# Optimization experiments

Measured on AMD Instinct MI355X. Metric: run time of the kernel, lower is better.

## Reference

```python
import jax, jax.numpy as jnp
import numpy as np

EPS = 1e-05
MARGIN = 0.0


def setup_inputs() -> dict:
    key = jax.random.key(0)
    k1, k2 = jax.random.split(key)
    embeddings = jax.random.normal(k1, (512, 512), dtype=jnp.float32)
    labels = jax.random.randint(k2, (512,), 0, 32, dtype=jnp.int64)
    return {"embeddings": embeddings, "labels": labels}


def _pairwise_distance(e, squared=False):
    # e: [B, D] -> [B, B] euclidean distances
    dot = jnp.matmul(e, e.T)
    sq = jnp.diag(dot)
    d = sq[:, None] - 2.0 * dot + sq[None, :]
    d = jnp.maximum(d, 0.0)
    if not squared:
        zmask = (d == 0.0).astype(d.dtype)
        d = d + zmask * EPS
        d = jnp.sqrt(d) + EPS
        d = d * (1.0 - zmask)
    return d


def _triplet_mask(labels):
    B = labels.shape[0]
    not_eq = ~jnp.eye(B, dtype=bool)
    # distinct indices i != j, i != k, j != k  -> [B, B, B]
    distinct = not_eq[:, :, None] & not_eq[:, None, :] & not_eq[None, :, :]
    lab_eq = labels[None, :] == labels[:, None]  # symmetric [B, B]
    valid = lab_eq[:, :, None] & (~lab_eq[:, None, :])  # label[i]==label[j], label[i]!=label[k]
    return (distinct & valid).astype(jnp.float32)


def reference(embeddings, labels):
    d = _pairwise_distance(embeddings, squared=False)  # [B, B]
    # triplet_loss[a, p, n] = d[a, p] - d[a, n] + margin
    tl = d[:, :, None] - d[:, None, :] + MARGIN
    mask = _triplet_mask(labels)
    tl = jnp.maximum(mask * tl, 0.0)
    num_positive = jnp.sum((tl > 1e-05).astype(jnp.float32))
    num_valid = jnp.sum(mask)
    fraction_positive = num_positive / (num_valid + 1e-05)
    loss = jnp.sum(tl) / (num_positive + 1e-05)
    return (loss, fraction_positive)
```

## Files before the change

### kernel.cpp

```cpp
#include <hip/hip_runtime.h>

#define BSZ 512
#define DIM 512
#define EPSF 1e-5f

__global__ __launch_bounds__(64) void norms_kernel(const float* __restrict__ E,
                                                   float* __restrict__ sq) {
    const int row = blockIdx.x;
    const int lane = threadIdx.x;
    const float4* rp = (const float4*)(E + (size_t)row * DIM);
    float4 a = rp[lane];
    float4 b = rp[lane + 64];
    float s = a.x*a.x + a.y*a.y + a.z*a.z + a.w*a.w
            + b.x*b.x + b.y*b.y + b.z*b.z + b.w*b.w;
#pragma unroll
    for (int off = 32; off > 0; off >>= 1) s += __shfl_down(s, off);
    if (lane == 0) sq[row] = s;
}

__device__ __forceinline__ float dist_xform(float sa, float sb, float dot) {
    float v = sa - 2.0f * dot + sb;
    v = fmaxf(v, 0.0f);
    float z = (v == 0.0f) ? 1.0f : 0.0f;
    v = sqrtf(v + z * EPSF) + EPSF;
    return v * (1.0f - z);
}

__global__ __launch_bounds__(256) void dist_kernel(const float* __restrict__ E,
                                                   const float* __restrict__ sq,
                                                   float* __restrict__ d) {
    __shared__ float As[32][33];
    __shared__ float Bs[32][33];
    const int bi = blockIdx.y * 32;
    const int bj = blockIdx.x * 32;
    const int tid = threadIdx.x;
    const int tx = tid & 15;
    const int ty = tid >> 4;
    const int lr = tid >> 3;
    const int lc = (tid & 7) * 4;

    float acc00 = 0.f, acc01 = 0.f, acc10 = 0.f, acc11 = 0.f;

    for (int k0 = 0; k0 < DIM; k0 += 32) {
        float4 av = *(const float4*)(E + (size_t)(bi + lr) * DIM + k0 + lc);
        float4 bv = *(const float4*)(E + (size_t)(bj + lr) * DIM + k0 + lc);
        As[lr][lc]   = av.x; As[lr][lc+1] = av.y; As[lr][lc+2] = av.z; As[lr][lc+3] = av.w;
        Bs[lr][lc]   = bv.x; Bs[lr][lc+1] = bv.y; Bs[lr][lc+2] = bv.z; Bs[lr][lc+3] = bv.w;
        __syncthreads();
#pragma unroll
        for (int kk = 0; kk < 32; ++kk) {
            float a0 = As[ty*2][kk],   a1 = As[ty*2+1][kk];
            float b0 = Bs[tx*2][kk],   b1 = Bs[tx*2+1][kk];
            acc00 += a0 * b0; acc01 += a0 * b1;
            acc10 += a1 * b0; acc11 += a1 * b1;
        }
        __syncthreads();
    }

    const int i0 = bi + ty * 2;
    const int j0 = bj + tx * 2;
    const float sqi0 = sq[i0], sqi1 = sq[i0+1];
    const float sqj0 = sq[j0], sqj1 = sq[j0+1];
    d[(size_t)i0*BSZ + j0]         = dist_xform(sqi0, sqj0, acc00);
    d[(size_t)i0*BSZ + j0+1]       = dist_xform(sqi0, sqj1, acc01);
    d[(size_t)(i0+1)*BSZ + j0]     = dist_xform(sqi1, sqj0, acc10);
    d[(size_t)(i0+1)*BSZ + j0+1]   = dist_xform(sqi1, sqj1, acc11);
}

__global__ __launch_bounds__(256) void triplet_kernel(const float* __restrict__ d,
                                                      const int* __restrict__ labels,
                                                      float* __restrict__ partial) {
    const int a = blockIdx.x;
    const int tid = threadIdx.x;
    __shared__ float drow[BSZ];
    __shared__ int   lab[BSZ];
    __shared__ int   poslist[BSZ];
    __shared__ int   npos_s;

    if (tid == 0) npos_s = 0;
    for (int t = tid; t < BSZ; t += 256) {
        lab[t]  = labels[t];
        drow[t] = d[(size_t)a * BSZ + t];
    }
    __syncthreads();

    const int la = lab[a];
    for (int t = tid; t < BSZ; t += 256) {
        if (lab[t] == la && t != a) {
            int idx = atomicAdd(&npos_s, 1);
            poslist[idx] = t;
        }
    }
    __syncthreads();

    const int npos = npos_s;
    const int nneg = BSZ - 1 - npos;
    float sum = 0.0f;
    int   cnt = 0;
    const int total = npos * BSZ;
    for (int idx = tid; idx < total; idx += 256) {
        const int p = poslist[idx >> 9];
        const int n = idx & (BSZ - 1);
        if (lab[n] != la) {
            const float v = drow[p] - drow[n];
            if (v > 0.0f)  sum += v;
            if (v > 1e-5f) cnt++;
        }
    }

#pragma unroll
    for (int off = 32; off > 0; off >>= 1) {
        sum += __shfl_down(sum, off);
        cnt += __shfl_down(cnt, off);
    }
    __shared__ float wsum[4];
    __shared__ int   wcnt[4];
    const int wave = tid >> 6, lane = tid & 63;
    if (lane == 0) { wsum[wave] = sum; wcnt[wave] = cnt; }
    __syncthreads();
    if (tid == 0) {
        float S = wsum[0] + wsum[1] + wsum[2] + wsum[3];
        int   C = wcnt[0] + wcnt[1] + wcnt[2] + wcnt[3];
        partial[a]            = S;
        partial[BSZ + a]      = (float)C;
        partial[2*BSZ + a]    = (float)npos * (float)nneg;
    }
}

__global__ __launch_bounds__(256) void final_kernel(const float* __restrict__ partial,
                                                    float* __restrict__ out) {
    const int tid = threadIdx.x;
    float s = partial[tid]         + partial[tid + 256];
    float c = partial[BSZ + tid]   + partial[BSZ + tid + 256];
    float v = partial[2*BSZ + tid] + partial[2*BSZ + tid + 256];
#pragma unroll
    for (int off = 32; off > 0; off >>= 1) {
        s += __shfl_down(s, off);
        c += __shfl_down(c, off);
        v += __shfl_down(v, off);
    }
    __shared__ float ws[4], wc[4], wv[4];
    const int wave = tid >> 6, lane = tid & 63;
    if (lane == 0) { ws[wave] = s; wc[wave] = c; wv[wave] = v; }
    __syncthreads();
    if (tid == 0) {
        float S = ws[0] + ws[1] + ws[2] + ws[3];
        float C = wc[0] + wc[1] + wc[2] + wc[3];
        float V = wv[0] + wv[1] + wv[2] + wv[3];
        out[0] = S / (C + 1e-5f);
        out[1] = C / (V + 1e-5f);
    }
}

extern "C" void kernel_launch(void* const* d_in, const int* in_sizes, int n_in,
                              void* d_out, int out_size, void* d_ws, size_t ws_size,
                              hipStream_t stream) {
    const float* E      = (const float*)d_in[0];
    const int*   labels = (const int*)d_in[1];
    float* out = (float*)d_out;

    float* sq      = (float*)d_ws;
    float* d       = sq + BSZ;
    float* partial = d + (size_t)BSZ * BSZ;

    norms_kernel<<<BSZ, 64, 0, stream>>>(E, sq);
    dist_kernel<<<dim3(16, 16), 256, 0, stream>>>(E, sq, d);
    triplet_kernel<<<BSZ, 256, 0, stream>>>(d, labels, partial);
    final_kernel<<<1, 256, 0, stream>>>(partial, out);
}
```

Measured before the change: 85.78 us.

## Fuse distance computation and triplet reduction into one kernel per anchor pair

```diff
diff --git a/kernel.cpp b/kernel.cpp
--- a/kernel.cpp
+++ b/kernel.cpp
@@ -1,100 +1,32 @@
 #include <hip/hip_runtime.h>
 
 #define BSZ 512
-#define DIM 512
 #define EPSF 1e-5f
 
-__global__ __launch_bounds__(64) void norms_kernel(const float* __restrict__ E,
-                                                   float* __restrict__ sq) {
-    const int row = blockIdx.x;
-    const int lane = threadIdx.x;
-    const float4* rp = (const float4*)(E + (size_t)row * DIM);
-    float4 a = rp[lane];
-    float4 b = rp[lane + 64];
-    float s = a.x*a.x + a.y*a.y + a.z*a.z + a.w*a.w
-            + b.x*b.x + b.y*b.y + b.z*b.z + b.w*b.w;
-#pragma unroll
-    for (int off = 32; off > 0; off >>= 1) s += __shfl_down(s, off);
-    if (lane == 0) sq[row] = s;
-}
-
-__device__ __forceinline__ float dist_xform(float sa, float sb, float dot) {
-    float v = sa - 2.0f * dot + sb;
+__device__ __forceinline__ float dist_xform(float v) {
     v = fmaxf(v, 0.0f);
     float z = (v == 0.0f) ? 1.0f : 0.0f;
     v = sqrtf(v + z * EPSF) + EPSF;
     return v * (1.0f - z);
 }
 
-__global__ __launch_bounds__(256) void dist_kernel(const float* __restrict__ E,
-                                                   const float* __restrict__ sq,
-                                                   float* __restrict__ d) {
-    __shared__ float As[32][33];
-    __shared__ float Bs[32][33];
-    const int bi = blockIdx.y * 32;
-    const int bj = blockIdx.x * 32;
-    const int tid = threadIdx.x;
-    const int tx = tid & 15;
-    const int ty = tid >> 4;
-    const int lr = tid >> 3;
-    const int lc = (tid & 7) * 4;
-
-    float acc00 = 0.f, acc01 = 0.f, acc10 = 0.f, acc11 = 0.f;
-
-    for (int k0 = 0; k0 < DIM; k0 += 32) {
-        float4 av = *(const float4*)(E + (size_t)(bi + lr) * DIM + k0 + lc);
-        float4 bv = *(const float4*)(E + (size_t)(bj + lr) * DIM + k0 + lc);
-        As[lr][lc]   = av.x; As[lr][lc+1] = av.y; As[lr][lc+2] = av.z; As[lr][lc+3] = av.w;
-        Bs[lr][lc]   = bv.x; Bs[lr][lc+1] = bv.y; Bs[lr][lc+2] = bv.z; Bs[lr][lc+3] = bv.w;
-        __syncthreads();
-#pragma unroll
-        for (int kk = 0; kk < 32; ++kk) {
-            float a0 = As[ty*2][kk],   a1 = As[ty*2+1][kk];
-            float b0 = Bs[tx*2][kk],   b1 = Bs[tx*2+1][kk];
-            acc00 += a0 * b0; acc01 += a0 * b1;
-            acc10 += a1 * b0; acc11 += a1 * b1;
-        }
-        __syncthreads();
-    }
-
-    const int i0 = bi + ty * 2;
-    const int j0 = bj + tx * 2;
-    const float sqi0 = sq[i0], sqi1 = sq[i0+1];
-    const float sqj0 = sq[j0], sqj1 = sq[j0+1];
-    d[(size_t)i0*BSZ + j0]         = dist_xform(sqi0, sqj0, acc00);
-    d[(size_t)i0*BSZ + j0+1]       = dist_xform(sqi0, sqj1, acc01);
-    d[(size_t)(i0+1)*BSZ + j0]     = dist_xform(sqi1, sqj0, acc10);
-    d[(size_t)(i0+1)*BSZ + j0+1]   = dist_xform(sqi1, sqj1, acc11);
-}
-
-__global__ __launch_bounds__(256) void triplet_kernel(const float* __restrict__ d,
-                                                      const int* __restrict__ labels,
-                                                      float* __restrict__ partial) {
-    const int a = blockIdx.x;
-    const int tid = threadIdx.x;
-    __shared__ float drow[BSZ];
-    __shared__ int   lab[BSZ];
-    __shared__ int   poslist[BSZ];
-    __shared__ int   npos_s;
-
-    if (tid == 0) npos_s = 0;
-    for (int t = tid; t < BSZ; t += 256) {
-        lab[t]  = labels[t];
-        drow[t] = d[(size_t)a * BSZ + t];
-    }
+__device__ __forceinline__ void triplet_phase(int a, const float* drow,
+                                              const int* lab, int* poslist,
+                                              int* npos_s, float* wsum, int* wcnt,
+                                              float* __restrict__ partial, int tid) {
+    if (tid == 0) *npos_s = 0;
     __syncthreads();
-
     const int la = lab[a];
     for (int t = tid; t < BSZ; t += 256) {
         if (lab[t] == la && t != a) {
-            int idx = atomicAdd(&npos_s, 1);
+            int idx = atomicAdd(npos_s, 1);
             poslist[idx] = t;
         }
     }
     __syncthreads();
+    const int npos = *npos_s;
+    const int nneg = BSZ - 1 - npos;
 
-    const int npos = npos_s;
-    const int nneg = BSZ - 1 - npos;
     float sum = 0.0f;
     int   cnt = 0;
     const int total = npos * BSZ;
@@ -107,24 +39,75 @@
             if (v > 1e-5f) cnt++;
         }
     }
-
 #pragma unroll
     for (int off = 32; off > 0; off >>= 1) {
         sum += __shfl_down(sum, off);
         cnt += __shfl_down(cnt, off);
     }
-    __shared__ float wsum[4];
-    __shared__ int   wcnt[4];
     const int wave = tid >> 6, lane = tid & 63;
     if (lane == 0) { wsum[wave] = sum; wcnt[wave] = cnt; }
     __syncthreads();
     if (tid == 0) {
-        float S = wsum[0] + wsum[1] + wsum[2] + wsum[3];
-        int   C = wcnt[0] + wcnt[1] + wcnt[2] + wcnt[3];
-        partial[a]            = S;
-        partial[BSZ + a]      = (float)C;
-        partial[2*BSZ + a]    = (float)npos * (float)nneg;
+        partial[a]           = wsum[0] + wsum[1] + wsum[2] + wsum[3];
+        partial[BSZ + a]     = (float)(wcnt[0] + wcnt[1] + wcnt[2] + wcnt[3]);
+        partial[2*BSZ + a]   = (float)npos * (float)nneg;
     }
+    __syncthreads();
+}
+
+__global__ __launch_bounds__(256) void fused_kernel(const float* __restrict__ E,
+                                                    const int* __restrict__ labels,
+                                                    float* __restrict__ partial) {
+    const int tid = threadIdx.x;
+    const int g = tid >> 3;
+    const int l = tid & 7;
+    const int a0 = blockIdx.x;
+    const int a1 = blockIdx.x + 256;
+
+    __shared__ float drow0[BSZ];
+    __shared__ float drow1[BSZ];
+    __shared__ int   lab[BSZ];
+    __shared__ int   poslist[BSZ];
+    __shared__ int   npos_s;
+    __shared__ float wsum[4];
+    __shared__ int   wcnt[4];
+
+    for (int t = tid; t < BSZ; t += 256) lab[t] = labels[t];
+
+    const float4* ra0 = (const float4*)(E + (size_t)a0 * BSZ);
+    const float4* ra1 = (const float4*)(E + (size_t)a1 * BSZ);
+    float4 e0[16], e1[16];
+#pragma unroll
+    for (int c = 0; c < 16; ++c) { e0[c] = ra0[c * 8 + l]; e1[c] = ra1[c * 8 + l]; }
+
+    for (int j0 = 0; j0 < BSZ; j0 += 32) {
+        const int j = j0 + g;
+        const float4* rj = (const float4*)(E + (size_t)j * BSZ);
+        float s0 = 0.0f, s1 = 0.0f;
+#pragma unroll
+        for (int c = 0; c < 16; ++c) {
+            float4 v = rj[c * 8 + l];
+            float d;
+            d = e0[c].x - v.x; s0 += d * d;
+            d = e0[c].y - v.y; s0 += d * d;
+            d = e0[c].z - v.z; s0 += d * d;
+            d = e0[c].w - v.w; s0 += d * d;
+            d = e1[c].x - v.x; s1 += d * d;
+            d = e1[c].y - v.y; s1 += d * d;
+            d = e1[c].z - v.z; s1 += d * d;
+            d = e1[c].w - v.w; s1 += d * d;
+        }
+        s0 += __shfl_xor(s0, 4); s0 += __shfl_xor(s0, 2); s0 += __shfl_xor(s0, 1);
+        s1 += __shfl_xor(s1, 4); s1 += __shfl_xor(s1, 2); s1 += __shfl_xor(s1, 1);
+        if (l == 0) {
+            drow0[j] = dist_xform(s0);
+            drow1[j] = dist_xform(s1);
+        }
+    }
+    __syncthreads();
+
+    triplet_phase(a0, drow0, lab, poslist, &npos_s, wsum, wcnt, partial, tid);
+    triplet_phase(a1, drow1, lab, poslist, &npos_s, wsum, wcnt, partial, tid);
 }
 
 __global__ __launch_bounds__(256) void final_kernel(const float* __restrict__ partial,
@@ -159,12 +142,8 @@
     const int*   labels = (const int*)d_in[1];
     float* out = (float*)d_out;
 
-    float* sq      = (float*)d_ws;
-    float* d       = sq + BSZ;
-    float* partial = d + (size_t)BSZ * BSZ;
+    float* partial = (float*)d_ws;
 
-    norms_kernel<<<BSZ, 64, 0, stream>>>(E, sq);
-    dist_kernel<<<dim3(16, 16), 256, 0, stream>>>(E, sq, d);
-    triplet_kernel<<<BSZ, 256, 0, stream>>>(d, labels, partial);
+    fused_kernel<<<256, 256, 0, stream>>>(E, labels, partial);
     final_kernel<<<1, 256, 0, stream>>>(partial, out);
 }
```

Result: slower. 156.8 us (+82.8%).
